# Kernel optimization log

Measured on AMD Instinct MI355X. Metric: run time of the kernel, lower is better.

## Reference

```python
import jax, jax.numpy as jnp
import numpy as np

ALPHA = 0.2  # LeakyReLU negative slope
NEG_BIG = -9e15

def setup_inputs() -> dict:
    key = jax.random.key(0)
    k1, k2, k3, k4 = jax.random.split(key, 4)
    B, N, Fin, Fout = 32, 1024, 64, 64
    x = jax.random.normal(k1, (B, N, Fin), dtype=jnp.float32)
    adj = jax.random.randint(k2, (B, N, N), 0, 2, dtype=jnp.int32)
    W = jax.random.normal(k3, (Fin, Fout), dtype=jnp.float32) * (1.414 / np.sqrt(Fin))
    a = jax.random.normal(k4, (2 * Fout, 1), dtype=jnp.float32) * 0.1
    return {"x": x, "adj": adj, "W": W, "a": a}

def reference(x, adj, W, a):
    # x: [B,N,Fin], adj: [B,N,N], W: [Fin,Fout], a: [2*Fout,1]
    h = jnp.einsum('bnf,fo->bno', x, W)               # [B,N,Fout]
    Fout = W.shape[1]
    a1 = a[:Fout, 0]                                   # source half
    a2 = a[Fout:, 0]                                   # target half
    # e_ij = leakyrelu(a1.h_i + a2.h_j)  (equivalent to concat+matmul)
    f = h @ a1                                         # [B,N]
    g = h @ a2                                         # [B,N]
    e = jax.nn.leaky_relu(f[:, :, None] + g[:, None, :], ALPHA)  # [B,N,N]
    att = jnp.where(adj > 0, e, jnp.float32(NEG_BIG))
    att = jax.nn.softmax(att, axis=2)                  # dropout p=0, eval mode
    h_prime = jnp.einsum('bij,bjo->bio', att, h)       # [B,N,Fout]
    return jax.nn.elu(h_prime)                         # concat=True -> elu
```

## Files before the change

kernel.cpp:

```cpp
#include <hip/hip_runtime.h>
#include <hip/hip_bf16.h>
#include <hip/hip_fp16.h>

#define NN 1024
#define FD 64
#define BB 32

typedef __attribute__((ext_vector_type(4))) float    f32x4;
typedef __attribute__((ext_vector_type(8))) _Float16 f16x8;

static __device__ __forceinline__ unsigned short f2hu(float x) {
  _Float16 h = (_Float16)x;
  return __builtin_bit_cast(unsigned short, h);
}

__global__ __launch_bounds__(256) void gat_k1(
    const float* __restrict__ x, const float* __restrict__ W,
    const float* __restrict__ av, float* __restrict__ fv,
    float* __restrict__ gv, unsigned short* __restrict__ hT)
{
  __shared__ __align__(16) float Wl[FD * FD];
  __shared__ __align__(16) float xl[FD * 68];
  __shared__ __align__(16) unsigned short tl[FD * FD];
  __shared__ __align__(16) float al[2 * FD];

  const int tid = threadIdx.x;
  const int b   = blockIdx.x >> 4;
  const int n0  = (blockIdx.x & 15) << 6;

  if (tid < 32) ((f32x4*)al)[tid] = ((const f32x4*)av)[tid];
  {
    const int r  = tid >> 2;
    const int cb = (tid & 3) << 2;
    const f32x4* Wg = (const f32x4*)W;
    const f32x4* xg = (const f32x4*)(x + ((size_t)(b * NN + n0)) * FD);
#pragma unroll
    for (int k = 0; k < 4; ++k) {
      f32x4 wv = Wg[r * 16 + cb + k];
      f32x4 xv = xg[r * 16 + cb + k];
      *(f32x4*)(Wl + r * FD + ((cb + k) << 2)) = wv;
      *(f32x4*)(xl + r * 68 + ((cb + k) << 2)) = xv;
    }
  }
  __syncthreads();

  const int r  = tid >> 2;
  const int o0 = (tid & 3) << 4;
  float acc[16];
#pragma unroll
  for (int i = 0; i < 16; ++i) acc[i] = 0.f;

#pragma unroll 8
  for (int f = 0; f < FD; ++f) {
    float xv = xl[r * 68 + f];
    const f32x4* wr = (const f32x4*)(Wl + f * FD + o0);
#pragma unroll
    for (int c = 0; c < 4; ++c) {
      f32x4 wv = wr[c];
      acc[c * 4 + 0] += xv * wv.x;
      acc[c * 4 + 1] += xv * wv.y;
      acc[c * 4 + 2] += xv * wv.z;
      acc[c * 4 + 3] += xv * wv.w;
    }
  }

  float fp = 0.f, gp = 0.f;
#pragma unroll
  for (int i = 0; i < 16; ++i) {
    fp += acc[i] * al[o0 + i];
    gp += acc[i] * al[FD + o0 + i];
  }
  fp += __shfl_xor(fp, 1); fp += __shfl_xor(fp, 2);
  gp += __shfl_xor(gp, 1); gp += __shfl_xor(gp, 2);
  if ((tid & 3) == 0) {
    fv[b * NN + n0 + r] = fp;
    gv[b * NN + n0 + r] = gp;
  }

#pragma unroll
  for (int i = 0; i < 16; ++i) {
    int o  = o0 + i;
    int sw = (o ^ (o >> 3)) & 7;
    tl[o * FD + ((((r >> 3) ^ sw) << 3) | (r & 7))] = f2hu(acc[i]);
  }
  __syncthreads();
  {
    const int c2 = tid & 7;
#pragma unroll
    for (int hh = 0; hh < 2; ++hh) {
      int o  = (tid >> 3) + 32 * hh;
      int sw = (o ^ (o >> 3)) & 7;
      f32x4 v = *(const f32x4*)(tl + o * FD + ((c2 ^ sw) << 3));
      *(f32x4*)(hT + ((size_t)(b * FD + o)) * NN + n0 + c2 * 8) = v;
    }
  }
}

__global__ __launch_bounds__(256) void gat_k2(
    const int* __restrict__ adj, const float* __restrict__ fv,
    const float* __restrict__ gv, const unsigned short* __restrict__ hT,
    float* __restrict__ out)
{
  __shared__ __align__(16) unsigned short Pl[32 * FD];
  __shared__ __align__(16) unsigned short Hl[FD * FD];
  __shared__ __align__(16) float gl[NN];
  __shared__ float dLds[32];
  __shared__ float red[8];

  const int tid  = threadIdx.x;
  const int b    = blockIdx.x >> 5;
  const int i0   = (blockIdx.x & 31) << 5;
  const int lane = tid & 63, w = tid >> 6;
  const int q = tid >> 3, s = tid & 7;
  const int bN = b * NN;

  f32x4 g4 = *(const f32x4*)(gv + bN + tid * 4);
  *(f32x4*)(gl + tid * 4) = g4;
  float gm = fmaxf(fmaxf(g4.x, g4.y), fmaxf(g4.z, g4.w));
  float fm = fv[bN + i0 + (tid & 31)];
#pragma unroll
  for (int m = 1; m < 64; m <<= 1) {
    gm = fmaxf(gm, __shfl_xor(gm, m));
    fm = fmaxf(fm, __shfl_xor(fm, m));
  }
  if (lane == 0) { red[w * 2] = gm; red[w * 2 + 1] = fm; }
  const float fr = fv[bN + i0 + q];
  __syncthreads();
  gm = fmaxf(fmaxf(red[0], red[2]), fmaxf(red[4], red[6]));
  fm = fmaxf(fmaxf(red[1], red[3]), fmaxf(red[5], red[7]));
  const float sm = fm + gm;
  const float Cb = fmaxf(sm, 0.2f * sm);

  const int*            adjS = adj + ((size_t)(bN + i0 + q)) * NN + s * 4;
  const unsigned short* hTS  = hT + ((size_t)(b * FD + q)) * NN + s * 8;

  float dAcc = 0.f;
  f32x4 acc[2];
  acc[0] = (f32x4){0.f, 0.f, 0.f, 0.f};
  acc[1] = (f32x4){0.f, 0.f, 0.f, 0.f};

  int4 A_a0, A_a1, A_h0, A_h1;
  int4 B_a0, B_a1, B_h0, B_h1;

#define TLOAD(P, jt) do {                                \
    const int j0_ = (jt) << 6;                           \
    P##a0 = *(const int4*)(adjS + j0_);                  \
    P##a1 = *(const int4*)(adjS + j0_ + 32);             \
    P##h0 = *(const int4*)(hTS + j0_);                   \
    P##h1 = *(const int4*)(hTS + (size_t)32 * NN + j0_); \
  } while (0)

#define PQUAD(avv, gg, half) do {                                          \
    float e0 = fr + gg.x; e0 = fmaxf(e0, 0.2f * e0) - Cb;                  \
    float e1 = fr + gg.y; e1 = fmaxf(e1, 0.2f * e1) - Cb;                  \
    float e2 = fr + gg.z; e2 = fmaxf(e2, 0.2f * e2) - Cb;                  \
    float e3 = fr + gg.w; e3 = fmaxf(e3, 0.2f * e3) - Cb;                  \
    float p0 = (avv.x > 0) ? __expf(e0) : 0.f;                             \
    float p1 = (avv.y > 0) ? __expf(e1) : 0.f;                             \
    float p2 = (avv.z > 0) ? __expf(e2) : 0.f;                             \
    float p3 = (avv.w > 0) ? __expf(e3) : 0.f;                             \
    dAcc += (p0 + p1) + (p2 + p3);                                         \
    uint2 uv_;                                                             \
    uv_.x = (unsigned)f2hu(p0) | ((unsigned)f2hu(p1) << 16);               \
    uv_.y = (unsigned)f2hu(p2) | ((unsigned)f2hu(p3) << 16);               \
    *(uint2*)(Pl + q * FD +                                                \
        (((((half) << 2) + (s >> 1)) ^ (q & 7)) << 3) + ((s & 1) << 2)) = uv_; \
  } while (0)

#define TPROC(P, jt) do {                                                  \
    const int jg_ = (jt) << 6;                                             \
    f32x4 g0_ = *(const f32x4*)(gl + jg_ + s * 4);                         \
    f32x4 g1_ = *(const f32x4*)(gl + jg_ + 32 + s * 4);                    \
    PQUAD(P##a0, g0_, 0); PQUAD(P##a1, g1_, 1);                            \
    *(int4*)(Hl + q * FD + ((s ^ (q & 7)) << 3)) = P##h0;                  \
    *(int4*)(Hl + (q + 32) * FD + ((s ^ (q & 7)) << 3)) = P##h1;           \
  } while (0)

#define MSTEP() do {                                                       \
    const int m16_ = lane & 15, hi_ = lane >> 4;                           \
    const int ar_ = ((w & 1) << 4) + m16_;                                 \
    const f16x8 a0_ = *(const f16x8*)(Pl + ar_ * FD + (((hi_)     ^ (ar_ & 7)) << 3)); \
    const f16x8 a1_ = *(const f16x8*)(Pl + ar_ * FD + (((hi_ + 4) ^ (ar_ & 7)) << 3)); \
    _Pragma("unroll")                                                      \
    for (int n_ = 0; n_ < 2; ++n_) {                                       \
      const int o_ = ((w >> 1) << 5) + (n_ << 4) + m16_;                   \
      const f16x8 b0_ = *(const f16x8*)(Hl + o_ * FD + (((hi_)     ^ (o_ & 7)) << 3)); \
      const f16x8 b1_ = *(const f16x8*)(Hl + o_ * FD + (((hi_ + 4) ^ (o_ & 7)) << 3)); \
      acc[n_] = __builtin_amdgcn_mfma_f32_16x16x32_f16(a0_, b0_, acc[n_], 0, 0, 0);    \
      acc[n_] = __builtin_amdgcn_mfma_f32_16x16x32_f16(a1_, b1_, acc[n_], 0, 0, 0);    \
    }                                                                      \
  } while (0)

  TLOAD(A_, 0);
  for (int tt = 0; tt < 8; ++tt) {
    TLOAD(B_, 2 * tt + 1);
    TPROC(A_, 2 * tt);
    __syncthreads();
    MSTEP();
    __syncthreads();
    TLOAD(A_, (tt < 7) ? (2 * tt + 2) : 15);
    TPROC(B_, 2 * tt + 1);
    __syncthreads();
    MSTEP();
    __syncthreads();
  }

  dAcc += __shfl_xor(dAcc, 1);
  dAcc += __shfl_xor(dAcc, 2);
  dAcc += __shfl_xor(dAcc, 4);
  if (s == 0) dLds[q] = dAcc;
  __syncthreads();

  const int m16 = lane & 15, hi4 = lane >> 4;
  const int wr = (w & 1) << 4, wc = (w >> 1) << 5;
  float* outp = out + ((size_t)(bN + i0 + wr + hi4 * 4)) * FD + wc + m16;
#pragma unroll
  for (int rr = 0; rr < 4; ++rr) {
    float d   = dLds[wr + hi4 * 4 + rr];
    float inv = d > 0.f ? 1.f / d : 0.f;
#pragma unroll
    for (int n = 0; n < 2; ++n) {
      float v = acc[n][rr] * inv;
      v = v > 0.f ? v : (__expf(v) - 1.f);
      outp[(size_t)rr * FD + n * 16] = v;
    }
  }
#undef TLOAD
#undef PQUAD
#undef TPROC
#undef MSTEP
}

extern "C" void kernel_launch(void* const* d_in, const int* in_sizes, int n_in,
                              void* d_out, int out_size, void* d_ws, size_t ws_size,
                              hipStream_t stream) {
  const float* x   = (const float*)d_in[0];
  const int*   adj = (const int*)d_in[1];
  const float* W   = (const float*)d_in[2];
  const float* a   = (const float*)d_in[3];
  float* out = (float*)d_out;

  unsigned short* hT = (unsigned short*)d_ws;
  float* fv = (float*)((char*)d_ws + (size_t)BB * FD * NN * 2);
  float* gv = fv + (size_t)BB * NN;

  gat_k1<<<dim3(BB * 16), dim3(256), 0, stream>>>(x, W, a, fv, gv, hT);
  gat_k2<<<dim3(BB * 32), dim3(256), 0, stream>>>(adj, fv, gv, hT, out);
}
```

Baseline: 42.21 us.

## Pre-swizzle h into MFMA fragment layout and compute P in registers

The first kernel now writes h in fp16 directly in the per-lane B-fragment order used by the 16x16x32 MFMA. The attention kernel then loads operands straight from global memory into registers, with no LDS staging. Each wave builds its own P fragment from adj and g in registers, and blocks now cover 64 rows across all 64 output columns. This removes every __syncthreads and all LDS round trips in the main loop, and gets the row-sum reduction from shuffles. The cost is that each wave reloads the full h tile from global or L2 (four times per block), there are half as many blocks, and register pressure rises.

```diff
diff --git a/kernel.cpp b/kernel.cpp
--- a/kernel.cpp
+++ b/kernel.cpp
@@ -13,15 +13,18 @@
   _Float16 h = (_Float16)x;
   return __builtin_bit_cast(unsigned short, h);
 }
+static __device__ __forceinline__ f16x8 bch(int4 v) {
+  return __builtin_bit_cast(f16x8, v);
+}
 
 __global__ __launch_bounds__(256) void gat_k1(
     const float* __restrict__ x, const float* __restrict__ W,
     const float* __restrict__ av, float* __restrict__ fv,
-    float* __restrict__ gv, unsigned short* __restrict__ hT)
+    float* __restrict__ gv, unsigned short* __restrict__ hF)
 {
   __shared__ __align__(16) float Wl[FD * FD];
   __shared__ __align__(16) float xl[FD * 68];
-  __shared__ __align__(16) unsigned short tl[FD * FD];
+  __shared__ __align__(16) unsigned short tl[FD * 64];
   __shared__ __align__(16) float al[2 * FD];
 
   const int tid = threadIdx.x;
@@ -79,156 +82,141 @@
 
 #pragma unroll
   for (int i = 0; i < 16; ++i) {
-    int o  = o0 + i;
-    int sw = (o ^ (o >> 3)) & 7;
-    tl[o * FD + ((((r >> 3) ^ sw) << 3) | (r & 7))] = f2hu(acc[i]);
+    int o = o0 + i;
+    tl[o * 64 + ((((r >> 3) ^ (o & 7)) << 3) | (r & 7))] = f2hu(acc[i]);
   }
   __syncthreads();
+
   {
-    const int c2 = tid & 7;
+    const int jt = n0 >> 6;
 #pragma unroll
     for (int hh = 0; hh < 2; ++hh) {
-      int o  = (tid >> 3) + 32 * hh;
-      int sw = (o ^ (o >> 3)) & 7;
-      f32x4 v = *(const f32x4*)(tl + o * FD + ((c2 ^ sw) << 3));
-      *(f32x4*)(hT + ((size_t)(b * FD + o)) * NN + n0 + c2 * 8) = v;
+      int u = tid + (hh << 8);
+      int frag = u >> 6, l = u & 63;
+      int o = ((frag >> 1) << 4) + (l & 15);
+      int c = ((frag & 1) << 2) + (l >> 4);
+      int4 v = *(const int4*)(tl + o * 64 + ((c ^ (o & 7)) << 3));
+      *(int4*)(hF + ((((size_t)(b * 16 + jt)) * 8 + frag) * 64 + l) * 8) = v;
     }
   }
 }
 
 __global__ __launch_bounds__(256) void gat_k2(
     const int* __restrict__ adj, const float* __restrict__ fv,
-    const float* __restrict__ gv, const unsigned short* __restrict__ hT,
+    const float* __restrict__ gv, const unsigned short* __restrict__ hF,
     float* __restrict__ out)
 {
-  __shared__ __align__(16) unsigned short Pl[32 * FD];
-  __shared__ __align__(16) unsigned short Hl[FD * FD];
   __shared__ __align__(16) float gl[NN];
-  __shared__ float dLds[32];
-  __shared__ float red[8];
+  __shared__ float red[4];
 
   const int tid  = threadIdx.x;
-  const int b    = blockIdx.x >> 5;
-  const int i0   = (blockIdx.x & 31) << 5;
+  const int b    = blockIdx.x >> 4;
+  const int i0   = (blockIdx.x & 15) << 6;
   const int lane = tid & 63, w = tid >> 6;
-  const int q = tid >> 3, s = tid & 7;
-  const int bN = b * NN;
+  const int m16  = lane & 15, hi = lane >> 4;
+  const int bN   = b * NN;
 
   f32x4 g4 = *(const f32x4*)(gv + bN + tid * 4);
   *(f32x4*)(gl + tid * 4) = g4;
   float gm = fmaxf(fmaxf(g4.x, g4.y), fmaxf(g4.z, g4.w));
-  float fm = fv[bN + i0 + (tid & 31)];
+  float fm = fv[bN + i0 + lane];
 #pragma unroll
   for (int m = 1; m < 64; m <<= 1) {
     gm = fmaxf(gm, __shfl_xor(gm, m));
     fm = fmaxf(fm, __shfl_xor(fm, m));
   }
-  if (lane == 0) { red[w * 2] = gm; red[w * 2 + 1] = fm; }
-  const float fr = fv[bN + i0 + q];
+  if (lane == 0) red[w] = gm;
+  const float fr = fv[bN + i0 + w * 16 + m16];
   __syncthreads();
-  gm = fmaxf(fmaxf(red[0], red[2]), fmaxf(red[4], red[6]));
-  fm = fmaxf(fmaxf(red[1], red[3]), fmaxf(red[5], red[7]));
+  gm = fmaxf(fmaxf(red[0], red[1]), fmaxf(red[2], red[3]));
   const float sm = fm + gm;
   const float Cb = fmaxf(sm, 0.2f * sm);
 
-  const int*            adjS = adj + ((size_t)(bN + i0 + q)) * NN + s * 4;
-  const unsigned short* hTS  = hT + ((size_t)(b * FD + q)) * NN + s * 8;
+  const int*  adjP = adj + ((size_t)(bN + i0 + w * 16 + m16)) * NN + hi * 8;
+  const int4* hFb  = (const int4*)hF + (size_t)b * 8192 + lane;
 
   float dAcc = 0.f;
-  f32x4 acc[2];
-  acc[0] = (f32x4){0.f, 0.f, 0.f, 0.f};
-  acc[1] = (f32x4){0.f, 0.f, 0.f, 0.f};
-
-  int4 A_a0, A_a1, A_h0, A_h1;
-  int4 B_a0, B_a1, B_h0, B_h1;
-
-#define TLOAD(P, jt) do {                                \
-    const int j0_ = (jt) << 6;                           \
-    P##a0 = *(const int4*)(adjS + j0_);                  \
-    P##a1 = *(const int4*)(adjS + j0_ + 32);             \
-    P##h0 = *(const int4*)(hTS + j0_);                   \
-    P##h1 = *(const int4*)(hTS + (size_t)32 * NN + j0_); \
+  f32x4 acc[4];
+#pragma unroll
+  for (int n = 0; n < 4; ++n) acc[n] = (f32x4){0.f, 0.f, 0.f, 0.f};
+
+  int4 Aa0, Aa1, Aa2, Aa3, Ba0, Ba1, Ba2, Ba3;
+
+#define LADJ(P, t) do { const int o_ = (t) << 6;        \
+    P##0 = *(const int4*)(adjP + o_);                   \
+    P##1 = *(const int4*)(adjP + o_ + 4);               \
+    P##2 = *(const int4*)(adjP + o_ + 32);              \
+    P##3 = *(const int4*)(adjP + o_ + 36); } while (0)
+
+#define PCOMP(dst, ia, ib, ga, gb) do {                                    \
+    float e0 = fr + ga.x, e1 = fr + ga.y, e2 = fr + ga.z, e3 = fr + ga.w;  \
+    float e4 = fr + gb.x, e5 = fr + gb.y, e6 = fr + gb.z, e7 = fr + gb.w;  \
+    e0 = fmaxf(e0, 0.2f * e0) - Cb; e1 = fmaxf(e1, 0.2f * e1) - Cb;        \
+    e2 = fmaxf(e2, 0.2f * e2) - Cb; e3 = fmaxf(e3, 0.2f * e3) - Cb;        \
+    e4 = fmaxf(e4, 0.2f * e4) - Cb; e5 = fmaxf(e5, 0.2f * e5) - Cb;        \
+    e6 = fmaxf(e6, 0.2f * e6) - Cb; e7 = fmaxf(e7, 0.2f * e7) - Cb;        \
+    float p0 = (ia.x > 0) ? __expf(e0) : 0.f;                              \
+    float p1 = (ia.y > 0) ? __expf(e1) : 0.f;                              \
+    float p2 = (ia.z > 0) ? __expf(e2) : 0.f;                              \
+    float p3 = (ia.w > 0) ? __expf(e3) : 0.f;                              \
+    float p4 = (ib.x > 0) ? __expf(e4) : 0.f;                              \
+    float p5 = (ib.y > 0) ? __expf(e5) : 0.f;                              \
+    float p6 = (ib.z > 0) ? __expf(e6) : 0.f;                              \
+    float p7 = (ib.w > 0) ? __expf(e7) : 0.f;                              \
+    dAcc += ((p0 + p1) + (p2 + p3)) + ((p4 + p5) + (p6 + p7));             \
+    dst = (f16x8){(_Float16)p0, (_Float16)p1, (_Float16)p2, (_Float16)p3,  \
+                  (_Float16)p4, (_Float16)p5, (_Float16)p6, (_Float16)p7}; \
   } while (0)
 
-#define PQUAD(avv, gg, half) do {                                          \
-    float e0 = fr + gg.x; e0 = fmaxf(e0, 0.2f * e0) - Cb;                  \
-    float e1 = fr + gg.y; e1 = fmaxf(e1, 0.2f * e1) - Cb;                  \
-    float e2 = fr + gg.z; e2 = fmaxf(e2, 0.2f * e2) - Cb;                  \
-    float e3 = fr + gg.w; e3 = fmaxf(e3, 0.2f * e3) - Cb;                  \
-    float p0 = (avv.x > 0) ? __expf(e0) : 0.f;                             \
-    float p1 = (avv.y > 0) ? __expf(e1) : 0.f;                             \
-    float p2 = (avv.z > 0) ? __expf(e2) : 0.f;                             \
-    float p3 = (avv.w > 0) ? __expf(e3) : 0.f;                             \
-    dAcc += (p0 + p1) + (p2 + p3);                                         \
-    uint2 uv_;                                                             \
-    uv_.x = (unsigned)f2hu(p0) | ((unsigned)f2hu(p1) << 16);               \
-    uv_.y = (unsigned)f2hu(p2) | ((unsigned)f2hu(p3) << 16);               \
-    *(uint2*)(Pl + q * FD +                                                \
-        (((((half) << 2) + (s >> 1)) ^ (q & 7)) << 3) + ((s & 1) << 2)) = uv_; \
+#define TILE(P, t) do {                                                    \
+    const int jb_ = (t) << 6;                                              \
+    const int4* hp_ = hFb + (size_t)(t) * 512;                             \
+    int4 h0_ = hp_[0],   h1_ = hp_[64],  h2_ = hp_[128], h3_ = hp_[192];   \
+    int4 h4_ = hp_[256], h5_ = hp_[320], h6_ = hp_[384], h7_ = hp_[448];   \
+    f32x4 ga0_ = *(const f32x4*)(gl + jb_ + hi * 8);                       \
+    f32x4 ga1_ = *(const f32x4*)(gl + jb_ + hi * 8 + 4);                   \
+    f32x4 gb0_ = *(const f32x4*)(gl + jb_ + 32 + hi * 8);                  \
+    f32x4 gb1_ = *(const f32x4*)(gl + jb_ + 32 + hi * 8 + 4);              \
+    f16x8 pa_, pb_;                                                        \
+    PCOMP(pa_, P##0, P##1, ga0_, ga1_);                                    \
+    PCOMP(pb_, P##2, P##3, gb0_, gb1_);                                    \
+    acc[0] = __builtin_amdgcn_mfma_f32_16x16x32_f16(pa_, bch(h0_), acc[0], 0, 0, 0); \
+    acc[0] = __builtin_amdgcn_mfma_f32_16x16x32_f16(pb_, bch(h1_), acc[0], 0, 0, 0); \
+    acc[1] = __builtin_amdgcn_mfma_f32_16x16x32_f16(pa_, bch(h2_), acc[1], 0, 0, 0); \
+    acc[1] = __builtin_amdgcn_mfma_f32_16x16x32_f16(pb_, bch(h3_), acc[1], 0, 0, 0); \
+    acc[2] = __builtin_amdgcn_mfma_f32_16x16x32_f16(pa_, bch(h4_), acc[2], 0, 0, 0); \
+    acc[2] = __builtin_amdgcn_mfma_f32_16x16x32_f16(pb_, bch(h5_), acc[2], 0, 0, 0); \
+    acc[3] = __builtin_amdgcn_mfma_f32_16x16x32_f16(pa_, bch(h6_), acc[3], 0, 0, 0); \
+    acc[3] = __builtin_amdgcn_mfma_f32_16x16x32_f16(pb_, bch(h7_), acc[3], 0, 0, 0); \
   } while (0)
 
-#define TPROC(P, jt) do {                                                  \
-    const int jg_ = (jt) << 6;                                             \
-    f32x4 g0_ = *(const f32x4*)(gl + jg_ + s * 4);                         \
-    f32x4 g1_ = *(const f32x4*)(gl + jg_ + 32 + s * 4);                    \
-    PQUAD(P##a0, g0_, 0); PQUAD(P##a1, g1_, 1);                            \
-    *(int4*)(Hl + q * FD + ((s ^ (q & 7)) << 3)) = P##h0;                  \
-    *(int4*)(Hl + (q + 32) * FD + ((s ^ (q & 7)) << 3)) = P##h1;           \
-  } while (0)
-
-#define MSTEP() do {                                                       \
-    const int m16_ = lane & 15, hi_ = lane >> 4;                           \
-    const int ar_ = ((w & 1) << 4) + m16_;                                 \
-    const f16x8 a0_ = *(const f16x8*)(Pl + ar_ * FD + (((hi_)     ^ (ar_ & 7)) << 3)); \
-    const f16x8 a1_ = *(const f16x8*)(Pl + ar_ * FD + (((hi_ + 4) ^ (ar_ & 7)) << 3)); \
-    _Pragma("unroll")                                                      \
-    for (int n_ = 0; n_ < 2; ++n_) {                                       \
-      const int o_ = ((w >> 1) << 5) + (n_ << 4) + m16_;                   \
-      const f16x8 b0_ = *(const f16x8*)(Hl + o_ * FD + (((hi_)     ^ (o_ & 7)) << 3)); \
-      const f16x8 b1_ = *(const f16x8*)(Hl + o_ * FD + (((hi_ + 4) ^ (o_ & 7)) << 3)); \
-      acc[n_] = __builtin_amdgcn_mfma_f32_16x16x32_f16(a0_, b0_, acc[n_], 0, 0, 0);    \
-      acc[n_] = __builtin_amdgcn_mfma_f32_16x16x32_f16(a1_, b1_, acc[n_], 0, 0, 0);    \
-    }                                                                      \
-  } while (0)
-
-  TLOAD(A_, 0);
+  LADJ(Aa, 0);
   for (int tt = 0; tt < 8; ++tt) {
-    TLOAD(B_, 2 * tt + 1);
-    TPROC(A_, 2 * tt);
-    __syncthreads();
-    MSTEP();
-    __syncthreads();
-    TLOAD(A_, (tt < 7) ? (2 * tt + 2) : 15);
-    TPROC(B_, 2 * tt + 1);
-    __syncthreads();
-    MSTEP();
-    __syncthreads();
-  }
-
-  dAcc += __shfl_xor(dAcc, 1);
-  dAcc += __shfl_xor(dAcc, 2);
-  dAcc += __shfl_xor(dAcc, 4);
-  if (s == 0) dLds[q] = dAcc;
-  __syncthreads();
-
-  const int m16 = lane & 15, hi4 = lane >> 4;
-  const int wr = (w & 1) << 4, wc = (w >> 1) << 5;
-  float* outp = out + ((size_t)(bN + i0 + wr + hi4 * 4)) * FD + wc + m16;
+    LADJ(Ba, 2 * tt + 1);
+    TILE(Aa, 2 * tt);
+    if (tt < 7) LADJ(Aa, 2 * tt + 2);
+    TILE(Ba, 2 * tt + 1);
+  }
+
+  dAcc += __shfl_xor(dAcc, 16);
+  dAcc += __shfl_xor(dAcc, 32);
+
+  float* outB = out + ((size_t)(bN + i0 + w * 16)) * FD;
 #pragma unroll
   for (int rr = 0; rr < 4; ++rr) {
-    float d   = dLds[wr + hi4 * 4 + rr];
+    const int lr = hi * 4 + rr;
+    float d   = __shfl(dAcc, lr);
     float inv = d > 0.f ? 1.f / d : 0.f;
 #pragma unroll
-    for (int n = 0; n < 2; ++n) {
+    for (int n = 0; n < 4; ++n) {
       float v = acc[n][rr] * inv;
       v = v > 0.f ? v : (__expf(v) - 1.f);
-      outp[(size_t)rr * FD + n * 16] = v;
-    }
-  }
-#undef TLOAD
-#undef PQUAD
-#undef TPROC
-#undef MSTEP
+      outB[(size_t)lr * FD + n * 16 + m16] = v;
+    }
+  }
+#undef LADJ
+#undef PCOMP
+#undef TILE
 }
 
 extern "C" void kernel_launch(void* const* d_in, const int* in_sizes, int n_in,
@@ -240,10 +228,10 @@
   const float* a   = (const float*)d_in[3];
   float* out = (float*)d_out;
 
-  unsigned short* hT = (unsigned short*)d_ws;
+  unsigned short* hF = (unsigned short*)d_ws;
   float* fv = (float*)((char*)d_ws + (size_t)BB * FD * NN * 2);
   float* gv = fv + (size_t)BB * NN;
 
-  gat_k1<<<dim3(BB * 16), dim3(256), 0, stream>>>(x, W, a, fv, gv, hT);
-  gat_k2<<<dim3(BB * 32), dim3(256), 0, stream>>>(adj, fv, gv, hT, out);
-}
+  gat_k1<<<dim3(BB * 16), dim3(256), 0, stream>>>(x, W, a, fv, gv, hF);
+  gat_k2<<<dim3(BB * 16), dim3(256), 0, stream>>>(adj, fv, gv, hF, out);
+}
```

Measured after the change: 44.30 us. 1.05x slower.

## Double-buffer LDS tiles in gat_k2 with one barrier per tile and staggered starts

Applied to the files above, without the earlier changes.

The P and H shared-memory tiles are now double-buffered, so each 64-column tile needs one barrier instead of two, using a raw s_barrier after an LDS waitcnt. Global loads for tile t+2 are issued right after the current tile is written to LDS. Each block starts at a rotated tile offset, which spreads concurrent adj/hT reads across memory, and the 16-tile loop is fully unrolled. The cost is double the LDS for P/H and more register pressure from unrolling, which could lower occupancy.

```diff
diff --git a/kernel.cpp b/kernel.cpp
--- a/kernel.cpp
+++ b/kernel.cpp
@@ -101,8 +101,8 @@
     const float* __restrict__ gv, const unsigned short* __restrict__ hT,
     float* __restrict__ out)
 {
-  __shared__ __align__(16) unsigned short Pl[32 * FD];
-  __shared__ __align__(16) unsigned short Hl[FD * FD];
+  __shared__ __align__(16) unsigned short Pl[2][32 * 64];
+  __shared__ __align__(16) unsigned short Hl[2][64 * 64];
   __shared__ __align__(16) float gl[NN];
   __shared__ float dLds[32];
   __shared__ float red[8];
@@ -110,6 +110,7 @@
   const int tid  = threadIdx.x;
   const int b    = blockIdx.x >> 5;
   const int i0   = (blockIdx.x & 31) << 5;
+  const int st   = blockIdx.x & 15;
   const int lane = tid & 63, w = tid >> 6;
   const int q = tid >> 3, s = tid & 7;
   const int bN = b * NN;
@@ -139,18 +140,15 @@
   acc[0] = (f32x4){0.f, 0.f, 0.f, 0.f};
   acc[1] = (f32x4){0.f, 0.f, 0.f, 0.f};
 
-  int4 A_a0, A_a1, A_h0, A_h1;
-  int4 B_a0, B_a1, B_h0, B_h1;
-
-#define TLOAD(P, jt) do {                                \
-    const int j0_ = (jt) << 6;                           \
-    P##a0 = *(const int4*)(adjS + j0_);                  \
-    P##a1 = *(const int4*)(adjS + j0_ + 32);             \
-    P##h0 = *(const int4*)(hTS + j0_);                   \
-    P##h1 = *(const int4*)(hTS + (size_t)32 * NN + j0_); \
-  } while (0)
-
-#define PQUAD(avv, gg, half) do {                                          \
+  int4 Aa0, Aa1, Ah0, Ah1, Ba0, Ba1, Bh0, Bh1;
+
+#define TLOAD(Ra0, Ra1, Rh0, Rh1, jt) do { const int j0_ = (jt) << 6; \
+    Ra0 = *(const int4*)(adjS + j0_);                                 \
+    Ra1 = *(const int4*)(adjS + j0_ + 32);                            \
+    Rh0 = *(const int4*)(hTS + j0_);                                  \
+    Rh1 = *(const int4*)(hTS + (size_t)32 * NN + j0_); } while (0)
+
+#define PQUAD(avv, gg, half, p) do {                                       \
     float e0 = fr + gg.x; e0 = fmaxf(e0, 0.2f * e0) - Cb;                  \
     float e1 = fr + gg.y; e1 = fmaxf(e1, 0.2f * e1) - Cb;                  \
     float e2 = fr + gg.z; e2 = fmaxf(e2, 0.2f * e2) - Cb;                  \
@@ -163,47 +161,50 @@
     uint2 uv_;                                                             \
     uv_.x = (unsigned)f2hu(p0) | ((unsigned)f2hu(p1) << 16);               \
     uv_.y = (unsigned)f2hu(p2) | ((unsigned)f2hu(p3) << 16);               \
-    *(uint2*)(Pl + q * FD +                                                \
+    *(uint2*)(Pl[p] + q * 64 +                                             \
         (((((half) << 2) + (s >> 1)) ^ (q & 7)) << 3) + ((s & 1) << 2)) = uv_; \
   } while (0)
 
-#define TPROC(P, jt) do {                                                  \
-    const int jg_ = (jt) << 6;                                             \
-    f32x4 g0_ = *(const f32x4*)(gl + jg_ + s * 4);                         \
-    f32x4 g1_ = *(const f32x4*)(gl + jg_ + 32 + s * 4);                    \
-    PQUAD(P##a0, g0_, 0); PQUAD(P##a1, g1_, 1);                            \
-    *(int4*)(Hl + q * FD + ((s ^ (q & 7)) << 3)) = P##h0;                  \
-    *(int4*)(Hl + (q + 32) * FD + ((s ^ (q & 7)) << 3)) = P##h1;           \
-  } while (0)
-
-#define MSTEP() do {                                                       \
+#define MSTEP(p) do {                                                      \
     const int m16_ = lane & 15, hi_ = lane >> 4;                           \
     const int ar_ = ((w & 1) << 4) + m16_;                                 \
-    const f16x8 a0_ = *(const f16x8*)(Pl + ar_ * FD + (((hi_)     ^ (ar_ & 7)) << 3)); \
-    const f16x8 a1_ = *(const f16x8*)(Pl + ar_ * FD + (((hi_ + 4) ^ (ar_ & 7)) << 3)); \
+    const f16x8 a0_ = *(const f16x8*)(Pl[p] + ar_ * 64 + (((hi_)     ^ (ar_ & 7)) << 3)); \
+    const f16x8 a1_ = *(const f16x8*)(Pl[p] + ar_ * 64 + (((hi_ + 4) ^ (ar_ & 7)) << 3)); \
     _Pragma("unroll")                                                      \
     for (int n_ = 0; n_ < 2; ++n_) {                                       \
       const int o_ = ((w >> 1) << 5) + (n_ << 4) + m16_;                   \
-      const f16x8 b0_ = *(const f16x8*)(Hl + o_ * FD + (((hi_)     ^ (o_ & 7)) << 3)); \
-      const f16x8 b1_ = *(const f16x8*)(Hl + o_ * FD + (((hi_ + 4) ^ (o_ & 7)) << 3)); \
-      acc[n_] = __builtin_amdgcn_mfma_f32_16x16x32_f16(a0_, b0_, acc[n_], 0, 0, 0);    \
-      acc[n_] = __builtin_amdgcn_mfma_f32_16x16x32_f16(a1_, b1_, acc[n_], 0, 0, 0);    \
+      const f16x8 b0_ = *(const f16x8*)(Hl[p] + o_ * 64 + (((hi_)     ^ (o_ & 7)) << 3)); \
+      const f16x8 b1_ = *(const f16x8*)(Hl[p] + o_ * 64 + (((hi_ + 4) ^ (o_ & 7)) << 3)); \
+      acc[n_] = __builtin_amdgcn_mfma_f32_16x16x32_f16(a0_, b0_, acc[n_], 0, 0, 0);       \
+      acc[n_] = __builtin_amdgcn_mfma_f32_16x16x32_f16(a1_, b1_, acc[n_], 0, 0, 0);       \
     }                                                                      \
   } while (0)
 
-  TLOAD(A_, 0);
-  for (int tt = 0; tt < 8; ++tt) {
-    TLOAD(B_, 2 * tt + 1);
-    TPROC(A_, 2 * tt);
-    __syncthreads();
-    MSTEP();
-    __syncthreads();
-    TLOAD(A_, (tt < 7) ? (2 * tt + 2) : 15);
-    TPROC(B_, 2 * tt + 1);
-    __syncthreads();
-    MSTEP();
-    __syncthreads();
-  }
+#define TILE_ONE(t, Ra0, Ra1, Rh0, Rh1, p) do {                            \
+    const int jt_ = ((t) + st) & 15;                                       \
+    const int jg_ = jt_ << 6;                                              \
+    f32x4 g0_ = *(const f32x4*)(gl + jg_ + s * 4);                         \
+    f32x4 g1_ = *(const f32x4*)(gl + jg_ + 32 + s * 4);                    \
+    PQUAD(Ra0, g0_, 0, p); PQUAD(Ra1, g1_, 1, p);                          \
+    *(int4*)(Hl[p] + q * 64 + ((s ^ (q & 7)) << 3)) = Rh0;                 \
+    *(int4*)(Hl[p] + (q + 32) * 64 + ((s ^ (q & 7)) << 3)) = Rh1;          \
+    if ((t) + 2 < 16) TLOAD(Ra0, Ra1, Rh0, Rh1, (((t) + 2 + st) & 15));    \
+    asm volatile("s_waitcnt lgkmcnt(0)" ::: "memory");                     \
+    __builtin_amdgcn_s_barrier();                                          \
+    MSTEP(p);                                                              \
+  } while (0)
+
+  TLOAD(Aa0, Aa1, Ah0, Ah1, st);
+  TLOAD(Ba0, Ba1, Bh0, Bh1, (st + 1) & 15);
+#pragma unroll
+  for (int t = 0; t < 16; t += 2) {
+    TILE_ONE(t,     Aa0, Aa1, Ah0, Ah1, 0);
+    TILE_ONE(t + 1, Ba0, Ba1, Bh0, Bh1, 1);
+  }
+#undef TLOAD
+#undef PQUAD
+#undef MSTEP
+#undef TILE_ONE
 
   dAcc += __shfl_xor(dAcc, 1);
   dAcc += __shfl_xor(dAcc, 2);
@@ -225,10 +226,6 @@
       outp[(size_t)rr * FD + n * 16] = v;
     }
   }
-#undef TLOAD
-#undef PQUAD
-#undef TPROC
-#undef MSTEP
 }
 
 extern "C" void kernel_launch(void* const* d_in, const int* in_sizes, int n_in,
```

Result: slower. 44.58 us (+5.6%).
